# Optimization experiments

Measured on AMD Instinct MI355X. Metric: run time of the kernel, lower is better.

The kernel has to match this reference:

```python
import jax, jax.numpy as jnp
import numpy as np

EPS = 1e-6


def setup_inputs() -> dict:
    key = jax.random.key(0)
    ks = jax.random.split(key, 7)
    T, B, D, N = 512, 32, 1024, 128
    scale_w = (6.0 / (N + D)) ** 0.5  # xavier_uniform bound
    def w(k):
        return jax.random.uniform(k, (N, D), jnp.float32, -scale_w, scale_w)
    return {
        "x": jax.random.normal(ks[0], (T, B, D), jnp.float32),
        "S0": jnp.zeros((B, N, N), jnp.float32),
        "W_k": w(ks[1]),
        "W_v": w(ks[2]),
        "W_q": w(ks[3]),
        "W_erase": w(ks[4]),
        "W_write": w(ks[5]),
    }


def _ntm_forward(x, S0, W_k, W_v, W_q, W_erase, W_write):
    # Projections for all timesteps at once: (T, B, n_state)
    k = jnp.einsum('tbd,nd->tbn', x, W_k)
    v = jnp.einsum('tbd,nd->tbn', x, W_v)
    q = jnp.einsum('tbd,nd->tbn', x, W_q)
    erase = jnp.einsum('tbd,nd->tbn', x, W_erase)  # use_sigmoid=False: raw
    write = jnp.einsum('tbd,nd->tbn', x, W_write)

    def step(S, inp):
        k_t, v_t, q_t, e_t, w_t = inp
        k_norm = k_t / (jnp.linalg.norm(k_t, axis=-1, keepdims=True) + EPS)
        # S: (B, n, n); outer products via broadcasting
        erase_outer = e_t[:, :, None] * k_norm[:, None, :]
        write_outer = (w_t * v_t)[:, :, None] * k_norm[:, None, :]
        S_new = jnp.tanh(S * (1.0 - erase_outer) + write_outer)
        Sq = jnp.einsum('bij,bj->bi', S_new, q_t)
        out = Sq * jax.nn.silu(Sq)
        return S_new, out

    S_final, outputs = jax.lax.scan(step, S0, (k, v, q, erase, write))
    return outputs, S_final


def reference(x, S0, W_k, W_v, W_q, W_erase, W_write):
    return _ntm_forward(x, S0, W_k, W_v, W_q, W_erase, W_write)
```

## Files before the change

### kernel.cpp

```cpp
#include <hip/hip_runtime.h>
#include <hip/hip_bf16.h>


typedef __attribute__((ext_vector_type(8))) short bf16x8;
typedef __attribute__((ext_vector_type(4))) float f32x4;
typedef __attribute__((ext_vector_type(2))) float f32x2;
typedef __attribute__((ext_vector_type(4))) unsigned short u16x4;
typedef __attribute__((ext_vector_type(8))) unsigned short u16x8;

static constexpr int T_STEPS = 512;
static constexpr int BATCH   = 32;
static constexpr int DDIM    = 1024;
static constexpr int NDIM    = 128;
static constexpr int LDC     = 5 * NDIM;
static constexpr int MROWS   = T_STEPS * BATCH;
static constexpr int OUT_N   = T_STEPS * BATCH * NDIM;

static constexpr size_t C_BYTES = (size_t)MROWS * LDC * 4;

__device__ __forceinline__ unsigned short rne_bf16(float v) {
    unsigned u = __builtin_bit_cast(unsigned, v);
    u += 0x7FFFu + ((u >> 16) & 1u);
    return (unsigned short)(u >> 16);
}

__global__ __launch_bounds__(256) void wconv_kernel(
    const float* __restrict__ w0, const float* __restrict__ w1,
    const float* __restrict__ w2, const float* __restrict__ w3,
    const float* __restrict__ w4,
    unsigned short* __restrict__ W2)
{
    const int idx = blockIdx.x * 256 + threadIdx.x;
    const size_t e = (size_t)idx * 4;
    const int bn = (int)(e >> 17);
    const int r  = (int)(e & 131071);
    const int n  = r >> 10;
    const int k  = r & 1023;

    const float* wp = w0;
    if (bn == 1) wp = w1;
    else if (bn == 2) wp = w2;
    else if (bn == 3) wp = w3;
    else if (bn == 4) wp = w4;

    f32x4 v = *(const f32x4*)(wp + r);
    u16x4 h;
#pragma unroll
    for (int j = 0; j < 4; ++j) h[j] = rne_bf16(v[j]);

    const int kk   = k >> 5;
    const int quad = (k >> 3) & 3;
    const size_t off = ((((size_t)(bn * 32 + kk) * 128 + n) * 4 + quad) * 8) + (k & 7);
    *(u16x4*)(W2 + off) = h;
}

template<int BN0, int NB>
__device__ __forceinline__ void gemm_pass(
    const unsigned short (&lds)[64 * 1024],
    const unsigned short* __restrict__ bp,
    float* __restrict__ C,
    int m0, int wave, int quad, int l16, int aswz)
{
    auto LDA = [&](int mi, int kk) -> bf16x8 {
        const int byteo = (mi * 16 + l16) * 2048 + ((kk * 64 + quad * 16) ^ aswz);
        return *(const bf16x8*)((const char*)lds + byteo);
    };

    f32x4 acc[NB][4];
#pragma unroll
    for (int q = 0; q < NB; ++q)
#pragma unroll
        for (int mi = 0; mi < 4; ++mi) acc[q][mi] = (f32x4)(0.0f);

    const unsigned short* bpp[NB];
#pragma unroll
    for (int q = 0; q < NB; ++q) bpp[q] = bp + (size_t)(BN0 + q) * 131072;

    bf16x8 aC[4], bC[NB], aN[4], bN[NB];
#pragma unroll
    for (int mi = 0; mi < 4; ++mi) aC[mi] = LDA(mi, 0);
#pragma unroll
    for (int q = 0; q < NB; ++q) bC[q] = *(const bf16x8*)bpp[q];

    for (int kk = 0; kk < 32; kk += 2) {
#pragma unroll
        for (int mi = 0; mi < 4; ++mi) aN[mi] = LDA(mi, kk + 1);
#pragma unroll
        for (int q = 0; q < NB; ++q)
            bN[q] = *(const bf16x8*)(bpp[q] + (size_t)(kk + 1) * 4096);
#pragma unroll
        for (int q = 0; q < NB; ++q)
#pragma unroll
            for (int mi = 0; mi < 4; ++mi)
                acc[q][mi] = __builtin_amdgcn_mfma_f32_16x16x32_bf16(
                    aC[mi], bC[q], acc[q][mi], 0, 0, 0);
        if (kk < 30) {
#pragma unroll
            for (int mi = 0; mi < 4; ++mi) aC[mi] = LDA(mi, kk + 2);
#pragma unroll
            for (int q = 0; q < NB; ++q)
                bC[q] = *(const bf16x8*)(bpp[q] + (size_t)(kk + 2) * 4096);
        }
#pragma unroll
        for (int q = 0; q < NB; ++q)
#pragma unroll
            for (int mi = 0; mi < 4; ++mi)
                acc[q][mi] = __builtin_amdgcn_mfma_f32_16x16x32_bf16(
                    aN[mi], bN[q], acc[q][mi], 0, 0, 0);
    }

#pragma unroll
    for (int q = 0; q < NB; ++q)
#pragma unroll
        for (int mi = 0; mi < 4; ++mi) {
            const int rw = m0 + mi * 16 + quad * 4;
            const int cl = (BN0 + q) * 128 + wave * 16 + l16;
#pragma unroll
            for (int r = 0; r < 4; ++r)
                C[(size_t)(rw + r) * LDC + cl] = acc[q][mi][r];
        }
}

__global__ __launch_bounds__(512, 2) void gemm5_kernel(
    const float* __restrict__ x,
    const unsigned short* __restrict__ W2,
    float* __restrict__ C)
{
    __shared__ unsigned short lds[64 * 1024];

    const int m0   = blockIdx.x * 64;
    const int tid  = threadIdx.x;
    const int wave = tid >> 6, lane = tid & 63;
    const int quad = lane >> 4, l16 = lane & 15;

    {
        const int k8 = tid & 127;
        const int rb = tid >> 7;
#pragma unroll 4
        for (int it = 0; it < 16; ++it) {
            const int row = it * 4 + rb;
            const float* src = x + (size_t)(m0 + row) * DDIM + k8 * 8;
            f32x4 v0 = *(const f32x4*)src;
            f32x4 v1 = *(const f32x4*)(src + 4);
            u16x8 h;
            h[0] = rne_bf16(v0[0]); h[1] = rne_bf16(v0[1]);
            h[2] = rne_bf16(v0[2]); h[3] = rne_bf16(v0[3]);
            h[4] = rne_bf16(v1[0]); h[5] = rne_bf16(v1[1]);
            h[6] = rne_bf16(v1[2]); h[7] = rne_bf16(v1[3]);
            const int byteo = row * 2048 + ((k8 * 16) ^ ((row & 7) << 4));
            *(u16x8*)((char*)lds + byteo) = h;
        }
    }
    __syncthreads();

    const int aswz = (l16 & 7) << 4;
    const unsigned short* bp = W2 + ((size_t)((wave * 16 + l16) * 4 + quad)) * 8;

    gemm_pass<0, 2>(lds, bp, C, m0, wave, quad, l16, aswz);
    gemm_pass<2, 2>(lds, bp, C, m0, wave, quad, l16, aswz);
    gemm_pass<4, 1>(lds, bp, C, m0, wave, quad, l16, aswz);
}

__global__ __launch_bounds__(256) void knorm_kernel(float* __restrict__ C)
{
    const int r    = blockIdx.x * 4 + (threadIdx.x >> 6);
    const int lane = threadIdx.x & 63;
    float* base = C + (size_t)r * LDC;

    f32x2 k2 = *(const f32x2*)(base + lane * 2);
    f32x2 v2 = *(const f32x2*)(base + NDIM + lane * 2);
    f32x2 w2 = *(const f32x2*)(base + 4 * NDIM + lane * 2);

    float ss = k2.x * k2.x + k2.y * k2.y;
#pragma unroll
    for (int off = 32; off >= 1; off >>= 1) ss += __shfl_xor(ss, off, 64);
    float inv = __builtin_amdgcn_rcpf(sqrtf(ss) + 1e-6f);

    f32x2 kn = {k2.x * inv, k2.y * inv};
    f32x2 wv = {v2.x * w2.x, v2.y * w2.y};
    *(f32x2*)(base + lane * 2) = kn;
    *(f32x2*)(base + NDIM + lane * 2) = wv;
}

__device__ __forceinline__ float tanh_fast(float xx) {
    float ex = __builtin_amdgcn_exp2f(xx * 2.8853900817779268f);
    float r  = __builtin_amdgcn_rcpf(ex + 1.0f);
    return fmaf(-2.0f, r, 1.0f);
}

template <int CTRL, int RMASK>
__device__ __forceinline__ float dpp_add(float x) {
    int yi = __builtin_amdgcn_update_dpp(
        0, __builtin_bit_cast(int, x), CTRL, RMASK, 0xF, true);
    return x + __builtin_bit_cast(float, yi);
}

__device__ __forceinline__ float dpp_reduce32(float x) {
    x = dpp_add<0xB1,  0xF>(x);
    x = dpp_add<0x4E,  0xF>(x);
    x = dpp_add<0x141, 0xF>(x);
    x = dpp_add<0x140, 0xF>(x);
    x = dpp_add<0x142, 0xA>(x);
    return x;
}

__global__ __launch_bounds__(256, 2) void ntm_scan_kernel(
    const float* __restrict__ C, const float* __restrict__ S0,
    float* __restrict__ out)
{
    const int L    = blockIdx.x;
    const int b    = (L & 7) + 8 * ((L >> 3) & 3);
    const int row  = (L >> 5) * 8 + (threadIdx.x >> 5);
    const int g    = threadIdx.x & 31;
    const int col0 = g * 4;

    f32x4 S = *(const f32x4*)(S0 + ((size_t)b * NDIM + row) * NDIM + col0);

    const size_t STRIDE = (size_t)BATCH * LDC;
    const float* pb = C + (size_t)b * LDC;

    f32x4 kS[4], qS[4];
    float eS[4], wvS[4];

#pragma unroll
    for (int s = 0; s < 2; ++s) {
        const float* p = pb + (size_t)s * STRIDE;
        kS[s]  = *(const f32x4*)(p + col0);
        qS[s]  = *(const f32x4*)(p + 2 * NDIM + col0);
        eS[s]  = p[3 * NDIM + row];
        wvS[s] = p[NDIM + row];
    }

    float* opc = out + (size_t)b * NDIM + row;
    const float* pc = pb + 2 * STRIDE;

    for (int ti = 0; ti < 127; ++ti) {
#pragma unroll
        for (int j = 0; j < 4; ++j) {
            const int ps = (j + 2) & 3;
            kS[ps]  = *(const f32x4*)(pc + col0);
            qS[ps]  = *(const f32x4*)(pc + 2 * NDIM + col0);
            eS[ps]  = pc[3 * NDIM + row];
            wvS[ps] = pc[NDIM + row];
            pc += STRIDE;

            float dot = 0.0f;
#pragma unroll
            for (int u = 0; u < 4; ++u) {
                float t0  = fmaf(-eS[j], S[u], wvS[j]);
                float pre = fmaf(kS[j][u], t0, S[u]);
                S[u] = tanh_fast(pre);
                dot = fmaf(S[u], qS[j][u], dot);
            }
            dot = dpp_reduce32(dot);

            if ((threadIdx.x & 31) == 31)
                *opc = dot;
            opc += BATCH * NDIM;
        }
    }

#pragma unroll
    for (int j = 0; j < 4; ++j) {
        const int ps = (j + 2) & 3;
        int tp = 510 + j;
        if (tp > T_STEPS - 1) tp = T_STEPS - 1;
        const float* p = pb + (size_t)tp * STRIDE;
        kS[ps]  = *(const f32x4*)(p + col0);
        qS[ps]  = *(const f32x4*)(p + 2 * NDIM + col0);
        eS[ps]  = p[3 * NDIM + row];
        wvS[ps] = p[NDIM + row];

        float dot = 0.0f;
#pragma unroll
        for (int u = 0; u < 4; ++u) {
            float t0  = fmaf(-eS[j], S[u], wvS[j]);
            float pre = fmaf(kS[j][u], t0, S[u]);
            S[u] = tanh_fast(pre);
            dot = fmaf(S[u], qS[j][u], dot);
        }
        dot = dpp_reduce32(dot);

        if ((threadIdx.x & 31) == 31)
            *opc = dot;
        opc += BATCH * NDIM;
    }

    *(f32x4*)(out + (size_t)T_STEPS * BATCH * NDIM
              + ((size_t)b * NDIM + row) * NDIM + col0) = S;
}

__global__ __launch_bounds__(256) void silu_kernel(float* __restrict__ out)
{
    const int i = blockIdx.x * 256 + threadIdx.x;
    f32x4 d = ((const f32x4*)out)[i];
    f32x4 y;
#pragma unroll
    for (int j = 0; j < 4; ++j) {
        float sg = __builtin_amdgcn_rcpf(
            1.0f + __builtin_amdgcn_exp2f(-d[j] * 1.4426950408889634f));
        y[j] = d[j] * d[j] * sg;
    }
    ((f32x4*)out)[i] = y;
}

extern "C" void kernel_launch(void* const* d_in, const int* in_sizes, int n_in,
                              void* d_out, int out_size, void* d_ws, size_t ws_size,
                              hipStream_t stream) {
    const float* x  = (const float*)d_in[0];
    const float* S0 = (const float*)d_in[1];
    const float* wk = (const float*)d_in[2];
    const float* wv = (const float*)d_in[3];
    const float* wq = (const float*)d_in[4];
    const float* we = (const float*)d_in[5];
    const float* ww = (const float*)d_in[6];
    float* out = (float*)d_out;
    float* C   = (float*)d_ws;
    unsigned short* W2 = (unsigned short*)((char*)d_ws + C_BYTES);

    wconv_kernel<<<640, 256, 0, stream>>>(wk, wv, wq, we, ww, W2);
    gemm5_kernel<<<256, 512, 0, stream>>>(x, W2, C);
    knorm_kernel<<<MROWS / 4, 256, 0, stream>>>(C);
    ntm_scan_kernel<<<512, 256, 0, stream>>>(C, S0, out);
    silu_kernel<<<OUT_N / 1024, 256, 0, stream>>>(out);
}
```

Before: 261.5 us.

## Fuse key normalization and write-value product into GEMM epilogue

```diff
diff --git a/kernel.cpp b/kernel.cpp
--- a/kernel.cpp
+++ b/kernel.cpp
@@ -16,7 +16,7 @@
 static constexpr int MROWS   = T_STEPS * BATCH;
 static constexpr int OUT_N   = T_STEPS * BATCH * NDIM;
 
-static constexpr size_t C_BYTES = (size_t)MROWS * LDC * 4;
+static constexpr size_t C_BYTES  = (size_t)MROWS * LDC * 4;
 
 __device__ __forceinline__ unsigned short rne_bf16(float v) {
     unsigned u = __builtin_bit_cast(unsigned, v);
@@ -54,27 +54,22 @@
     *(u16x4*)(W2 + off) = h;
 }
 
-template<int BN0, int NB>
-__device__ __forceinline__ void gemm_pass(
-    const unsigned short (&lds)[64 * 1024],
-    const unsigned short* __restrict__ bp,
-    float* __restrict__ C,
-    int m0, int wave, int quad, int l16, int aswz)
+template<int NB>
+__device__ __forceinline__ void kloop(
+    const unsigned short* __restrict__ lds,
+    const unsigned short* const (&bpp)[NB],
+    int l16, int quad, int aswz,
+    f32x4 (&acc)[NB][4])
 {
     auto LDA = [&](int mi, int kk) -> bf16x8 {
         const int byteo = (mi * 16 + l16) * 2048 + ((kk * 64 + quad * 16) ^ aswz);
         return *(const bf16x8*)((const char*)lds + byteo);
     };
 
-    f32x4 acc[NB][4];
 #pragma unroll
     for (int q = 0; q < NB; ++q)
 #pragma unroll
         for (int mi = 0; mi < 4; ++mi) acc[q][mi] = (f32x4)(0.0f);
-
-    const unsigned short* bpp[NB];
-#pragma unroll
-    for (int q = 0; q < NB; ++q) bpp[q] = bp + (size_t)(BN0 + q) * 131072;
 
     bf16x8 aC[4], bC[NB], aN[4], bN[NB];
 #pragma unroll
@@ -108,25 +103,14 @@
                 acc[q][mi] = __builtin_amdgcn_mfma_f32_16x16x32_bf16(
                     aN[mi], bN[q], acc[q][mi], 0, 0, 0);
     }
-
-#pragma unroll
-    for (int q = 0; q < NB; ++q)
-#pragma unroll
-        for (int mi = 0; mi < 4; ++mi) {
-            const int rw = m0 + mi * 16 + quad * 4;
-            const int cl = (BN0 + q) * 128 + wave * 16 + l16;
-#pragma unroll
-            for (int r = 0; r < 4; ++r)
-                C[(size_t)(rw + r) * LDC + cl] = acc[q][mi][r];
-        }
-}
-
-__global__ __launch_bounds__(512, 2) void gemm5_kernel(
+}
+
+__global__ __launch_bounds__(512, 2) void gemm7_kernel(
     const float* __restrict__ x,
     const unsigned short* __restrict__ W2,
     float* __restrict__ C)
 {
-    __shared__ unsigned short lds[64 * 1024];
+    __shared__ unsigned short lds[64 * 1024 + 1024];
 
     const int m0   = blockIdx.x * 64;
     const int tid  = threadIdx.x;
@@ -155,31 +139,74 @@
 
     const int aswz = (l16 & 7) << 4;
     const unsigned short* bp = W2 + ((size_t)((wave * 16 + l16) * 4 + quad)) * 8;
-
-    gemm_pass<0, 2>(lds, bp, C, m0, wave, quad, l16, aswz);
-    gemm_pass<2, 2>(lds, bp, C, m0, wave, quad, l16, aswz);
-    gemm_pass<4, 1>(lds, bp, C, m0, wave, quad, l16, aswz);
-}
-
-__global__ __launch_bounds__(256) void knorm_kernel(float* __restrict__ C)
-{
-    const int r    = blockIdx.x * 4 + (threadIdx.x >> 6);
-    const int lane = threadIdx.x & 63;
-    float* base = C + (size_t)r * LDC;
-
-    f32x2 k2 = *(const f32x2*)(base + lane * 2);
-    f32x2 v2 = *(const f32x2*)(base + NDIM + lane * 2);
-    f32x2 w2 = *(const f32x2*)(base + 4 * NDIM + lane * 2);
-
-    float ss = k2.x * k2.x + k2.y * k2.y;
-#pragma unroll
-    for (int off = 32; off >= 1; off >>= 1) ss += __shfl_xor(ss, off, 64);
-    float inv = __builtin_amdgcn_rcpf(sqrtf(ss) + 1e-6f);
-
-    f32x2 kn = {k2.x * inv, k2.y * inv};
-    f32x2 wv = {v2.x * w2.x, v2.y * w2.y};
-    *(f32x2*)(base + lane * 2) = kn;
-    *(f32x2*)(base + NDIM + lane * 2) = wv;
+    float* lds2f = (float*)((char*)lds + 131072);
+
+    auto STORE = [&](int bn, const f32x4 (&a)[4]) {
+#pragma unroll
+        for (int mi = 0; mi < 4; ++mi) {
+            const int rw = m0 + mi * 16 + quad * 4;
+            const int cl = bn * 128 + wave * 16 + l16;
+#pragma unroll
+            for (int r = 0; r < 4; ++r)
+                C[(size_t)(rw + r) * LDC + cl] = a[mi][r];
+        }
+    };
+
+    f32x4 wv[4];
+    {
+        const unsigned short* bppVW[2] = { bp + 1 * 131072, bp + 4 * 131072 };
+        f32x4 acc[2][4];
+        kloop<2>(lds, bppVW, l16, quad, aswz, acc);
+#pragma unroll
+        for (int mi = 0; mi < 4; ++mi)
+#pragma unroll
+            for (int r = 0; r < 4; ++r)
+                wv[mi][r] = acc[0][mi][r] * acc[1][mi][r];
+    }
+
+    {
+        const unsigned short* bppKQ[2] = { bp, bp + 2 * 131072 };
+        f32x4 acc[2][4];
+        kloop<2>(lds, bppKQ, l16, quad, aswz, acc);
+
+#pragma unroll
+        for (int mi = 0; mi < 4; ++mi)
+#pragma unroll
+            for (int r = 0; r < 4; ++r) {
+                float s = acc[0][mi][r] * acc[0][mi][r];
+                s += __shfl_xor(s, 1);
+                s += __shfl_xor(s, 2);
+                s += __shfl_xor(s, 4);
+                s += __shfl_xor(s, 8);
+                if (l16 == 0)
+                    lds2f[(mi * 16 + quad * 4 + r) * 8 + wave] = s;
+            }
+        __syncthreads();
+
+#pragma unroll
+        for (int mi = 0; mi < 4; ++mi)
+#pragma unroll
+            for (int r = 0; r < 4; ++r) {
+                const int row = mi * 16 + quad * 4 + r;
+                f32x4 p0 = *(const f32x4*)&lds2f[row * 8];
+                f32x4 p1 = *(const f32x4*)&lds2f[row * 8 + 4];
+                float ss = (p0[0] + p0[1]) + (p0[2] + p0[3])
+                         + (p1[0] + p1[1]) + (p1[2] + p1[3]);
+                float inv = __builtin_amdgcn_rcpf(sqrtf(ss) + 1e-6f);
+                acc[0][mi][r] *= inv;
+            }
+
+        STORE(0, acc[0]);
+        STORE(1, wv);
+        STORE(2, acc[1]);
+    }
+
+    {
+        const unsigned short* bppE[1] = { bp + 3 * 131072 };
+        f32x4 acc[1][4];
+        kloop<1>(lds, bppE, l16, quad, aswz, acc);
+        STORE(3, acc[0]);
+    }
 }
 
 __device__ __forceinline__ float tanh_fast(float xx) {
@@ -319,8 +346,7 @@
     unsigned short* W2 = (unsigned short*)((char*)d_ws + C_BYTES);
 
     wconv_kernel<<<640, 256, 0, stream>>>(wk, wv, wq, we, ww, W2);
-    gemm5_kernel<<<256, 512, 0, stream>>>(x, W2, C);
-    knorm_kernel<<<MROWS / 4, 256, 0, stream>>>(C);
+    gemm7_kernel<<<256, 512, 0, stream>>>(x, W2, C);
     ntm_scan_kernel<<<512, 256, 0, stream>>>(C, S0, out);
     silu_kernel<<<OUT_N / 1024, 256, 0, stream>>>(out);
 }
```

Measured after the change: 270.0 us. 1.03x slower.
